# Kernel tuning notes

Hardware: AMD Instinct MI355X
Metric: run time of the kernel (lower is better)

The kernel has to match this reference:

```python
import jax, jax.numpy as jnp
import numpy as np
from math import log

D_MODEL = 512
MAX_LEN = 2048
B, S = 32, 2048


def make_pe(max_len, d_model):
    position = np.arange(max_len, dtype=np.float32)[:, None]
    div_term = np.exp(np.arange(0, d_model, 2, dtype=np.float32) * (-log(10000.0) / d_model))
    pe = np.zeros((max_len, d_model), dtype=np.float32)
    pe[:, 0::2] = np.sin(position * div_term)
    pe[:, 1::2] = np.cos(position * div_term)
    return jnp.asarray(pe)


def setup_inputs() -> dict:
    key = jax.random.key(0)
    k1, k2 = jax.random.split(key)
    seqs = jax.random.normal(k1, (B, S, D_MODEL), dtype=jnp.float32)
    masks = jax.random.randint(k2, (B, S), 0, 2) > 0
    pe = make_pe(MAX_LEN, D_MODEL)
    return {"seqs": seqs, "masks": masks, "pe": pe}


def reference(seqs, masks, pe):
    # Each masked (True) position in row i receives pe[r], where r is its rank
    # among the masked positions of that row (0-based). Equivalent to the
    # original per-sample loop: seq[masks[i]] += pe[:length].
    rank = jnp.cumsum(masks.astype(jnp.int32), axis=-1) - 1  # [B,S]
    rank = jnp.clip(rank, 0, pe.shape[0] - 1)
    p = pe[rank]  # [B,S,D] gather
    return seqs + jnp.where(masks[..., None], p, jnp.zeros((), seqs.dtype))
```

## Files before the change

### kernel.cpp

```cpp
#include <hip/hip_runtime.h>

#define BB 32
#define SS 2048
#define DD 512
#define VEC_PER_ROW (DD / 4)

__global__ void pe_rank_kernel(const unsigned int* __restrict__ m32,
                               int* __restrict__ rank_out) {
    const int b = blockIdx.x;
    const int t = threadIdx.x;

    __shared__ int flag_byte;
    if (t == 0) flag_byte = 0;
    __syncthreads();
    for (int i = t; i < 16384; i += 256) {
        unsigned int v = m32[i];
        if (v != 0u && v != 1u && v != 0x3f800000u) flag_byte = 1;
    }
    __syncthreads();
    const int is_byte = flag_byte;
    const unsigned char* m8 = (const unsigned char*)m32;

    __shared__ int psum[256];
    const int PER = SS / 256;
    int vals[PER];
    int s = 0;
#pragma unroll
    for (int i = 0; i < PER; ++i) {
        const int idx = b * SS + t * PER + i;
        const int mv = is_byte ? (m8[idx] != 0) : (m32[idx] != 0u);
        vals[i] = mv;
        s += mv;
    }
    psum[t] = s;
    __syncthreads();
    for (int off = 1; off < 256; off <<= 1) {
        const int v = (t >= off) ? psum[t - off] : 0;
        __syncthreads();
        psum[t] += v;
        __syncthreads();
    }
    int run = psum[t] - s;
#pragma unroll
    for (int i = 0; i < PER; ++i) {
        run += vals[i];
        rank_out[b * SS + t * PER + i] = vals[i] ? (run - 1) : -1;
    }
}

__global__ void pe_add_kernel(const float4* __restrict__ seqs,
                              const int* __restrict__ rank,
                              const float4* __restrict__ pe,
                              float4* __restrict__ out) {
    const int total = BB * SS * VEC_PER_ROW;
    const int stride = gridDim.x * blockDim.x;
    for (int idx = blockIdx.x * blockDim.x + threadIdx.x; idx < total;
         idx += stride) {
        const int row = idx >> 7;
        const int v   = idx & (VEC_PER_ROW - 1);
        float4 sv = seqs[idx];
        const int rk = rank[row];
        if (rk >= 0) {
            const float4 pv = pe[(rk << 7) + v];
            sv.x += pv.x;
            sv.y += pv.y;
            sv.z += pv.z;
            sv.w += pv.w;
        }
        out[idx] = sv;
    }
}

extern "C" void kernel_launch(void* const* d_in, const int* in_sizes, int n_in,
                              void* d_out, int out_size, void* d_ws, size_t ws_size,
                              hipStream_t stream) {
    const float* seqs        = (const float*)d_in[0];
    const unsigned int* msks = (const unsigned int*)d_in[1];
    const float* pe          = (const float*)d_in[2];
    float* out               = (float*)d_out;
    int* rank                = (int*)d_ws;

    pe_rank_kernel<<<BB, 256, 0, stream>>>(msks, rank);

    pe_add_kernel<<<2048, 256, 0, stream>>>(
        (const float4*)seqs, rank, (const float4*)pe, (float4*)out);
}
```

Measured before the change: 256.4 us.

## Unroll PE-add with batched loads, nontemporal IO, and widen rank scan block

Rewrites the add kernel as a fixed 16-iteration grid-stride loop, unrolled by four. It issues four seqs loads and four rank loads per group, so more memory requests are in flight. The row index is made wave-uniform through readfirstlane, so rank reads become scalar loads. Loads and stores of the streaming data are nontemporal, and the masked add is branchless: pe is always gathered and multiplied by a 0/1 factor. The rank kernel moves to 1024 threads per block and scans a smaller prefix when detecting the mask dtype. The branchless gather adds pe reads for unmasked rows, and the shorter dtype check rests on a heuristic.

```diff
diff --git a/kernel.cpp b/kernel.cpp
--- a/kernel.cpp
+++ b/kernel.cpp
@@ -3,17 +3,25 @@
 #define BB 32
 #define SS 2048
 #define DD 512
-#define VEC_PER_ROW (DD / 4)
+#define V4_PER_ROW (DD / 4)
+#define TOTAL (BB * SS * V4_PER_ROW)
+#define TPB 256
+#define GRID 2048
+#define STRIDE (GRID * TPB)
+#define ITERS (TOTAL / STRIDE)
+#define ROWSTEP (STRIDE / V4_PER_ROW)
 
-__global__ void pe_rank_kernel(const unsigned int* __restrict__ m32,
-                               int* __restrict__ rank_out) {
+typedef float f32x4 __attribute__((ext_vector_type(4)));
+
+__global__ __launch_bounds__(1024) void pe_rank_kernel(
+    const unsigned int* __restrict__ m32, int* __restrict__ rank_out) {
     const int b = blockIdx.x;
     const int t = threadIdx.x;
 
     __shared__ int flag_byte;
     if (t == 0) flag_byte = 0;
     __syncthreads();
-    for (int i = t; i < 16384; i += 256) {
+    for (int i = t; i < 8192; i += 1024) {
         unsigned int v = m32[i];
         if (v != 0u && v != 1u && v != 0x3f800000u) flag_byte = 1;
     }
@@ -21,8 +29,8 @@
     const int is_byte = flag_byte;
     const unsigned char* m8 = (const unsigned char*)m32;
 
-    __shared__ int psum[256];
-    const int PER = SS / 256;
+    __shared__ int psum[1024];
+    const int PER = SS / 1024;
     int vals[PER];
     int s = 0;
 #pragma unroll
@@ -34,7 +42,7 @@
     }
     psum[t] = s;
     __syncthreads();
-    for (int off = 1; off < 256; off <<= 1) {
+    for (int off = 1; off < 1024; off <<= 1) {
         const int v = (t >= off) ? psum[t - off] : 0;
         __syncthreads();
         psum[t] += v;
@@ -48,26 +56,45 @@
     }
 }
 
-__global__ void pe_add_kernel(const float4* __restrict__ seqs,
-                              const int* __restrict__ rank,
-                              const float4* __restrict__ pe,
-                              float4* __restrict__ out) {
-    const int total = BB * SS * VEC_PER_ROW;
-    const int stride = gridDim.x * blockDim.x;
-    for (int idx = blockIdx.x * blockDim.x + threadIdx.x; idx < total;
-         idx += stride) {
-        const int row = idx >> 7;
-        const int v   = idx & (VEC_PER_ROW - 1);
-        float4 sv = seqs[idx];
-        const int rk = rank[row];
-        if (rk >= 0) {
-            const float4 pv = pe[(rk << 7) + v];
-            sv.x += pv.x;
-            sv.y += pv.y;
-            sv.z += pv.z;
-            sv.w += pv.w;
-        }
-        out[idx] = sv;
+__global__ __launch_bounds__(TPB) void pe_add_kernel(
+    const f32x4* __restrict__ seqs, const int* __restrict__ rank,
+    const f32x4* __restrict__ pe, f32x4* __restrict__ out) {
+    const int tid = blockIdx.x * TPB + threadIdx.x;
+    const int col = tid & (V4_PER_ROW - 1);
+    const int rowbase = __builtin_amdgcn_readfirstlane(tid >> 7);
+
+#pragma unroll
+    for (int g = 0; g < ITERS / 4; ++g) {
+        const int k = 4 * g;
+        const int r0 = rank[rowbase + (k + 0) * ROWSTEP];
+        const int r1 = rank[rowbase + (k + 1) * ROWSTEP];
+        const int r2 = rank[rowbase + (k + 2) * ROWSTEP];
+        const int r3 = rank[rowbase + (k + 3) * ROWSTEP];
+        const f32x4 a0 = __builtin_nontemporal_load(&seqs[tid + (k + 0) * STRIDE]);
+        const f32x4 a1 = __builtin_nontemporal_load(&seqs[tid + (k + 1) * STRIDE]);
+        const f32x4 a2 = __builtin_nontemporal_load(&seqs[tid + (k + 2) * STRIDE]);
+        const f32x4 a3 = __builtin_nontemporal_load(&seqs[tid + (k + 3) * STRIDE]);
+        const int rc0 = r0 < 0 ? 0 : r0;
+        const int rc1 = r1 < 0 ? 0 : r1;
+        const int rc2 = r2 < 0 ? 0 : r2;
+        const int rc3 = r3 < 0 ? 0 : r3;
+        const f32x4 p0 = pe[(rc0 << 7) + col];
+        const f32x4 p1 = pe[(rc1 << 7) + col];
+        const f32x4 p2 = pe[(rc2 << 7) + col];
+        const f32x4 p3 = pe[(rc3 << 7) + col];
+        const float f0 = r0 < 0 ? 0.0f : 1.0f;
+        const float f1 = r1 < 0 ? 0.0f : 1.0f;
+        const float f2 = r2 < 0 ? 0.0f : 1.0f;
+        const float f3 = r3 < 0 ? 0.0f : 1.0f;
+        f32x4 o0, o1, o2, o3;
+        o0 = a0; o0 += p0 * f0;
+        o1 = a1; o1 += p1 * f1;
+        o2 = a2; o2 += p2 * f2;
+        o3 = a3; o3 += p3 * f3;
+        __builtin_nontemporal_store(o0, &out[tid + (k + 0) * STRIDE]);
+        __builtin_nontemporal_store(o1, &out[tid + (k + 1) * STRIDE]);
+        __builtin_nontemporal_store(o2, &out[tid + (k + 2) * STRIDE]);
+        __builtin_nontemporal_store(o3, &out[tid + (k + 3) * STRIDE]);
     }
 }
 
@@ -80,8 +107,7 @@
     float* out               = (float*)d_out;
     int* rank                = (int*)d_ws;
 
-    pe_rank_kernel<<<BB, 256, 0, stream>>>(msks, rank);
-
-    pe_add_kernel<<<2048, 256, 0, stream>>>(
-        (const float4*)seqs, rank, (const float4*)pe, (float4*)out);
+    pe_rank_kernel<<<BB, 1024, 0, stream>>>(msks, rank);
+    pe_add_kernel<<<GRID, TPB, 0, stream>>>(
+        (const f32x4*)seqs, rank, (const f32x4*)pe, (f32x4*)out);
 }
```

After: 244.6 us. 4.6% less time.
